# Kernel optimization log

Measured on AMD Instinct MI355X. Metric: run time of the kernel, lower is better.

## Reference

```python
import jax, jax.numpy as jnp
import numpy as np

T, B, D, H = 512, 64, 512, 512


def setup_inputs() -> dict:
    key = jax.random.key(0)
    ks = jax.random.split(key, 9)
    s_in = 1.0 / np.sqrt(D + H)  # nn.Linear default init scale
    inputs = jax.random.normal(ks[0], (T, B, D), dtype=jnp.float32)
    def lin(kw, kb):
        W = jax.random.uniform(kw, (D + H, H), jnp.float32, -s_in, s_in)
        b = jax.random.uniform(kb, (H,), jnp.float32, -s_in, s_in)
        return W, b
    W_f, b_f = lin(ks[1], ks[2])
    W_i, b_i = lin(ks[3], ks[4])
    W_g, b_g = lin(ks[5], ks[6])
    W_o, b_o = lin(ks[7], ks[8])
    return {"inputs": inputs, "W_f": W_f, "b_f": b_f, "W_i": W_i, "b_i": b_i,
            "W_g": W_g, "b_g": b_g, "W_o": W_o, "b_o": b_o}


def reference(inputs, W_f, b_f, W_i, b_i, W_g, b_g, W_o, b_o):
    # inputs: [T, B, D]; weights: [D+H, H]; gate_factory is identity (default)
    Bsz = inputs.shape[1]
    Hd = W_f.shape[1]
    # Fuse the 4 gate linears into one [D+H, 4H] GEMM per step (same math).
    W = jnp.concatenate([W_f, W_i, W_g, W_o], axis=1)  # [D+H, 4H]
    b = jnp.concatenate([b_f, b_i, b_g, b_o], axis=0)  # [4H]
    h0 = jnp.zeros((Bsz, Hd), dtype=inputs.dtype)
    c0 = jnp.zeros((Bsz, Hd), dtype=inputs.dtype)

    def step(carry, x):
        hx, cx = carry
        combined = jnp.concatenate([x, hx], axis=1)        # [B, D+H]
        gates = combined @ W + b                            # [B, 4H]
        f, i, g, o = jnp.split(gates, 4, axis=1)
        f = jax.nn.sigmoid(f)
        i = jax.nn.sigmoid(i)
        g = jnp.tanh(g)
        o = jax.nn.sigmoid(o)
        cx = f * cx + i * g
        hx = o * jnp.tanh(cx)
        return (hx, cx), hx

    (hx, cx), outputs = jax.lax.scan(step, (h0, c0), inputs)
    return outputs, (hx, cx)
```

## Files before the change

### kernel.cpp

```cpp
#include <hip/hip_runtime.h>

typedef unsigned int u32;
typedef unsigned short u16;
typedef __attribute__((ext_vector_type(8))) short bf16x8;
typedef __attribute__((ext_vector_type(4))) float f32x4;

#define T_STEPS 512
#define NOUT_H  16777216ull
#define WS_FLAGS  256ull
#define WS_BIAS   8192ull
#define WS_HBUF0  16384ull
#define WS_HBUF1  81920ull
#define WS_WXS    147456ull
#define WS_WHS    2244608ull
#define WS_XC     4341760ull
#define WS_XW     37896192ull

__device__ __forceinline__ u16 f2bf(float f) {
  u32 u = __builtin_bit_cast(u32, f);
  u32 r = (u + 0x7fffu + ((u >> 16) & 1u)) >> 16;
  return (u16)r;
}
__device__ __forceinline__ float bf2f(u16 h) {
  u32 u = ((u32)h) << 16;
  return __builtin_bit_cast(float, u);
}
__device__ __forceinline__ float sigf(float x) {
  return __builtin_amdgcn_rcpf(1.0f + __expf(-x));
}
__device__ __forceinline__ float tanh_fast(float x) {
  float xc = fminf(15.0f, fmaxf(-15.0f, x));
  float e = __expf(2.0f * xc);
  return (e - 1.0f) * __builtin_amdgcn_rcpf(e + 1.0f);
}

__global__ void k_detect(const u32* __restrict__ x, u32* __restrict__ ws) {
  __shared__ int cnt;
  if (threadIdx.x == 0) cnt = 0;
  __syncthreads();
  int good = 0;
  for (int i = 0; i < 4; ++i) {
    u32 v = x[threadIdx.x * 4 + i];
    u32 e = (v >> 7) & 0xff;
    good += (e >= 100 && e <= 140) ? 1 : 0;
  }
  atomicAdd(&cnt, good);
  __syncthreads();
  if (threadIdx.x == 0) ws[0] = (cnt >= 512) ? 1u : 0u;
  u32* flags = ws + WS_FLAGS / 4;
  for (int i = threadIdx.x; i < 1024; i += 256) flags[i] = 0;
  u32* hb = ws + WS_HBUF0 / 4;
  for (int i = threadIdx.x; i < (131072 / 4); i += 256) hb[i] = 0;
}

__global__ void k_convx(const u32* __restrict__ ws, const void* __restrict__ xin,
                        u16* __restrict__ xc) {
  if (ws[0]) return;
  int idx = blockIdx.x * 256 + threadIdx.x;
  float4 f = ((const float4*)xin)[idx];
  ushort4 o;
  o.x = f2bf(f.x); o.y = f2bf(f.y); o.z = f2bf(f.z); o.w = f2bf(f.w);
  ((ushort4*)xc)[idx] = o;
}

__global__ void k_prepw(u32* __restrict__ ws,
                        const void* Wf, const void* Wi, const void* Wg, const void* Wo,
                        const void* bfp, const void* bip, const void* bgp, const void* bop) {
  u32 mode = ws[0];
  const void* Wp[4] = {Wf, Wi, Wg, Wo};
  int tid = blockIdx.x * 256 + threadIdx.x;
  u16* wxs = (u16*)((char*)ws + WS_WXS);
  u16* whs = (u16*)((char*)ws + WS_WHS);
  int c, iswh;
  if (tid < 131072) { c = tid; iswh = 0; } else { c = tid - 131072; iswh = 1; }
  int n = c & 15, q = (c >> 4) & 3, ks = (c >> 6) & 15;
  int g, j, krow0;
  if (!iswh) {
    int ntg = c >> 10;
    int col = ntg * 16 + n; g = col >> 9; j = col & 511; krow0 = 0;
  } else {
    int nt = (c >> 10) & 1, w = c >> 11;
    int cl = nt * 16 + n; g = cl >> 3; j = w * 8 + (cl & 7); krow0 = 512;
  }
  int kbase = krow0 + ks * 32 + q * 8;
  u16 vals[8];
  if (mode) {
    const u16* Ws = (const u16*)Wp[g];
    for (int jj = 0; jj < 8; ++jj) vals[jj] = Ws[(size_t)(kbase + jj) * 512 + j];
  } else {
    const float* Ws = (const float*)Wp[g];
    for (int jj = 0; jj < 8; ++jj) vals[jj] = f2bf(Ws[(size_t)(kbase + jj) * 512 + j]);
  }
  uint4 pk;
  pk.x = (u32)vals[0] | ((u32)vals[1] << 16);
  pk.y = (u32)vals[2] | ((u32)vals[3] << 16);
  pk.z = (u32)vals[4] | ((u32)vals[5] << 16);
  pk.w = (u32)vals[6] | ((u32)vals[7] << 16);
  ((uint4*)(iswh ? whs : wxs))[c] = pk;
  if (tid < 2048) {
    const void* bp[4] = {bfp, bip, bgp, bop};
    int bg = tid >> 9, bj = tid & 511;
    float* bias = (float*)((char*)ws + WS_BIAS);
    bias[tid] = mode ? bf2f(((const u16*)bp[bg])[bj]) : ((const float*)bp[bg])[bj];
  }
}

__global__ __launch_bounds__(256) void k_xw(u32* __restrict__ ws, const void* __restrict__ xorig,
                                            int xwf32) {
  u32 mode = ws[0];
  const u16* xc = mode ? (const u16*)xorig : (const u16*)((char*)ws + WS_XC);
  const u16* wxs = (const u16*)((char*)ws + WS_WXS);
  const float* bias = (const float*)((char*)ws + WS_BIAS);
  char* xwp = (char*)ws + WS_XW;
  int v = threadIdx.x >> 6, lane = threadIdx.x & 63, q = lane >> 4, n = lane & 15;
  int mg = blockIdx.x >> 4, ng = blockIdx.x & 15;
  f32x4 acc[4][2] = {};
  for (int ks = 0; ks < 16; ++ks) {
    bf16x8 a[4];
#pragma unroll
    for (int mt = 0; mt < 4; ++mt)
      a[mt] = *(const bf16x8*)(xc + ((size_t)(mg * 64 + mt * 16 + n) * 512 + ks * 32 + q * 8));
#pragma unroll
    for (int jb = 0; jb < 2; ++jb) {
      int ntg = ng * 8 + v * 2 + jb;
      bf16x8 b = *(const bf16x8*)(wxs + ((size_t)(ntg * 16 + ks) * 64 + lane) * 8);
#pragma unroll
      for (int mt = 0; mt < 4; ++mt)
        acc[mt][jb] = __builtin_amdgcn_mfma_f32_16x16x32_bf16(a[mt], b, acc[mt][jb], 0, 0, 0);
    }
  }
#pragma unroll
  for (int jb = 0; jb < 2; ++jb) {
    int ntg = ng * 8 + v * 2 + jb;
    int col = ntg * 16 + n;
    float bv = bias[col];
    int g = col >> 9, j = col & 511;
    int w = j >> 3, cl = g * 8 + (j & 7);
    int nt4 = cl >> 4, n4 = cl & 15;
#pragma unroll
    for (int mt = 0; mt < 4; ++mt) {
      size_t base = ((((size_t)mg * 4 + mt) * 64 + w) * 2 + nt4) * 64 + q * 16 + n4;
      f32x4 vec = acc[mt][jb];
      vec[0] += bv; vec[1] += bv; vec[2] += bv; vec[3] += bv;
      if (xwf32) {
        ((f32x4*)xwp)[base] = vec;
      } else {
        ushort4 o;
        o.x = f2bf(vec[0]); o.y = f2bf(vec[1]); o.z = f2bf(vec[2]); o.w = f2bf(vec[3]);
        ((ushort4*)xwp)[base] = o;
      }
    }
  }
}

__global__ __launch_bounds__(256, 1) void k_rec(u32* __restrict__ ws, void* __restrict__ out,
                                                int xwf32) {
  __shared__ __align__(16) u16 whlds[16384];
  __shared__ float gbuf[4 * 16 * 33];
  __shared__ __align__(16) u16 houtbuf[64 * 8];
  u32 mode = ws[0];
  u32* flags = ws + WS_FLAGS / 4;
  const u16* whs = (const u16*)((char*)ws + WS_WHS);
  char* hb0 = (char*)ws + WS_HBUF0;
  char* hb1 = (char*)ws + WS_HBUF1;
  const char* xwp = (const char*)ws + WS_XW;
  int w = blockIdx.x, tid = threadIdx.x, v = tid >> 6, lane = tid & 63;
  int q = lane >> 4, n = lane & 15;

  {
    const uint4* src = (const uint4*)(whs + (size_t)w * 16384);
    uint4* dst = (uint4*)whlds;
    for (int i = tid; i < 2048; i += 256) dst[i] = src[i];
  }
  __syncthreads();

  float creg[2] = {0.f, 0.f};
  float* gb = &gbuf[v * 16 * 33];
  const u32* fp = flags + lane * 4;

  for (int t = 0; t < T_STEPS; ++t) {
    f32x4 xw0, xw1;
    {
      size_t b0 = ((((size_t)t * 4 + v) * 64 + w) * 2 + 0) * 64 + lane;
      if (xwf32) {
        xw0 = ((const f32x4*)xwp)[b0];
        xw1 = ((const f32x4*)xwp)[b0 + 64];
      } else {
        ushort4 a0 = ((const ushort4*)xwp)[b0];
        ushort4 a1 = ((const ushort4*)xwp)[b0 + 64];
        xw0[0] = bf2f(a0.x); xw0[1] = bf2f(a0.y); xw0[2] = bf2f(a0.z); xw0[3] = bf2f(a0.w);
        xw1[0] = bf2f(a1.x); xw1[1] = bf2f(a1.y); xw1[2] = bf2f(a1.z); xw1[3] = bf2f(a1.w);
      }
    }
    {
      u32 need = (u32)t;
      while (true) {
        uint4 f;
        asm volatile("global_load_dwordx4 %0, %1, off sc0 sc1\n\ts_waitcnt vmcnt(0)"
                     : "=&v"(f) : "v"(fp) : "memory");
        int ok = (f.x >= need) && (f.y >= need) && (f.z >= need) && (f.w >= need);
        if (__all(ok)) break;
        __builtin_amdgcn_s_sleep(1);
      }
    }
    const char* hcur = (t & 1) ? hb1 : hb0;
    char* hnxt = (t & 1) ? hb0 : hb1;

    uint4 ha[16];
    {
      const char* b0 = hcur + (size_t)v * 16384 + (size_t)lane * 16;
      const char* b4 = b0 + 4096;
      const char* b8 = b0 + 8192;
      const char* b12 = b0 + 12288;
      asm volatile(
          "global_load_dwordx4 %0, %16, off sc0 sc1\n\t"
          "global_load_dwordx4 %1, %16, off offset:1024 sc0 sc1\n\t"
          "global_load_dwordx4 %2, %16, off offset:2048 sc0 sc1\n\t"
          "global_load_dwordx4 %3, %16, off offset:3072 sc0 sc1\n\t"
          "global_load_dwordx4 %4, %17, off sc0 sc1\n\t"
          "global_load_dwordx4 %5, %17, off offset:1024 sc0 sc1\n\t"
          "global_load_dwordx4 %6, %17, off offset:2048 sc0 sc1\n\t"
          "global_load_dwordx4 %7, %17, off offset:3072 sc0 sc1\n\t"
          "global_load_dwordx4 %8, %18, off sc0 sc1\n\t"
          "global_load_dwordx4 %9, %18, off offset:1024 sc0 sc1\n\t"
          "global_load_dwordx4 %10, %18, off offset:2048 sc0 sc1\n\t"
          "global_load_dwordx4 %11, %18, off offset:3072 sc0 sc1\n\t"
          "global_load_dwordx4 %12, %19, off sc0 sc1\n\t"
          "global_load_dwordx4 %13, %19, off offset:1024 sc0 sc1\n\t"
          "global_load_dwordx4 %14, %19, off offset:2048 sc0 sc1\n\t"
          "global_load_dwordx4 %15, %19, off offset:3072 sc0 sc1\n\t"
          "s_waitcnt vmcnt(0)"
          : "=&v"(ha[0]), "=&v"(ha[1]), "=&v"(ha[2]), "=&v"(ha[3]),
            "=&v"(ha[4]), "=&v"(ha[5]), "=&v"(ha[6]), "=&v"(ha[7]),
            "=&v"(ha[8]), "=&v"(ha[9]), "=&v"(ha[10]), "=&v"(ha[11]),
            "=&v"(ha[12]), "=&v"(ha[13]), "=&v"(ha[14]), "=&v"(ha[15])
          : "v"(b0), "v"(b4), "v"(b8), "v"(b12)
          : "memory");
    }

    f32x4 acc0 = xw0, acc1 = xw1;
#pragma unroll
    for (int ks = 0; ks < 16; ++ks) {
      bf16x8 a = __builtin_bit_cast(bf16x8, ha[ks]);
      bf16x8 bb0 = *(const bf16x8*)&whlds[(ks * 64 + lane) * 8];
      bf16x8 bb1 = *(const bf16x8*)&whlds[((16 + ks) * 64 + lane) * 8];
      acc0 = __builtin_amdgcn_mfma_f32_16x16x32_bf16(a, bb0, acc0, 0, 0, 0);
      acc1 = __builtin_amdgcn_mfma_f32_16x16x32_bf16(a, bb1, acc1, 0, 0, 0);
    }
#pragma unroll
    for (int r = 0; r < 4; ++r) {
      gb[(q * 4 + r) * 33 + n] = acc0[r];
      gb[(q * 4 + r) * 33 + 16 + n] = acc1[r];
    }
    float hnew_s[2], cnew_s[2];
    int bidx[2];
#pragma unroll
    for (int it = 0; it < 2; ++it) {
      int item = it * 64 + lane, r16 = item >> 3, jj = item & 7, b = v * 16 + r16;
      float zf = gb[r16 * 33 + jj];
      float zi = gb[r16 * 33 + 8 + jj];
      float zg = gb[r16 * 33 + 16 + jj];
      float zo = gb[r16 * 33 + 24 + jj];
      float fg = sigf(zf), ig = sigf(zi), gg = tanh_fast(zg), og = sigf(zo);
      float cnew = fg * creg[it] + ig * gg;
      float hnew = og * tanh_fast(cnew);
      creg[it] = cnew;
      hnew_s[it] = hnew; cnew_s[it] = cnew; bidx[it] = b;
      houtbuf[b * 8 + jj] = f2bf(hnew);
    }
    if (lane < 16) {
      const u32* hv = (const u32*)&houtbuf[(v * 16 + lane) * 8];
      u32 v0 = hv[0], v1 = hv[1], v2 = hv[2], v3 = hv[3];
      size_t ci = (((size_t)v * 16 + (w >> 2)) * 4 + (w & 3)) * 16 + lane;
      void* dst = hnxt + ci * 16;
      asm volatile(
          "global_store_dword %0, %1, off sc0 sc1\n\t"
          "global_store_dword %0, %2, off offset:4 sc0 sc1\n\t"
          "global_store_dword %0, %3, off offset:8 sc0 sc1\n\t"
          "global_store_dword %0, %4, off offset:12 sc0 sc1"
          :: "v"(dst), "v"(v0), "v"(v1), "v"(v2), "v"(v3) : "memory");
    }
    asm volatile("s_waitcnt vmcnt(0)" ::: "memory");
    if (lane == 0) {
      u32 tag = (u32)(t + 1);
      u32* fdst = flags + (w * 4 + v);
      asm volatile("global_store_dword %0, %1, off sc0 sc1" :: "v"(fdst), "v"(tag) : "memory");
    }
#pragma unroll
    for (int it = 0; it < 2; ++it) {
      int item = it * 64 + lane, jj = item & 7, b = bidx[it];
      size_t oi = ((size_t)t * 64 + b) * 512 + w * 8 + jj;
      if (mode) ((u16*)out)[oi] = f2bf(hnew_s[it]); else ((float*)out)[oi] = hnew_s[it];
      if (t == T_STEPS - 1) {
        size_t hx = NOUT_H + (size_t)b * 512 + w * 8 + jj;
        if (mode) { ((u16*)out)[hx] = f2bf(hnew_s[it]); ((u16*)out)[hx + 32768] = f2bf(cnew_s[it]); }
        else      { ((float*)out)[hx] = hnew_s[it]; ((float*)out)[hx + 32768] = cnew_s[it]; }
      }
    }
  }
}

extern "C" void kernel_launch(void* const* d_in, const int* in_sizes, int n_in,
                              void* d_out, int out_size, void* d_ws, size_t ws_size,
                              hipStream_t stream) {
  const void* X = d_in[0];
  u32* ws = (u32*)d_ws;
  int xwf32 = (ws_size >= (size_t)(WS_XW + 268435456ull + 1024ull)) ? 1 : 0;

  k_detect<<<1, 256, 0, stream>>>((const u32*)X, ws);
  k_convx<<<16384, 256, 0, stream>>>(ws, X, (u16*)((char*)d_ws + WS_XC));
  k_prepw<<<1024, 256, 0, stream>>>(ws, d_in[1], d_in[3], d_in[5], d_in[7],
                                    d_in[2], d_in[4], d_in[6], d_in[8]);
  k_xw<<<8192, 256, 0, stream>>>(ws, X, xwf32);
  k_rec<<<64, 256, 0, stream>>>(ws, d_out, xwf32);
}
```

Baseline: 2.316 ms.

## Keep recurrent weights in registers, shuffle gates, and tighten per-step sync

The recurrent weight slice is held in VGPRs instead of LDS, and the gate values are exchanged between lanes with cross-lane shuffles, so the LDS staging buffers and their round trips go away. The MFMA chain is split into two independent accumulators to shorten the dependency chain. The flag poll now loads one dword per lane and no longer sleeps between polls. The next step's input projection is prefetched after the flag store, and h is written straight to global memory with short stores. The cost is much higher register pressure and more polling traffic on the flags.

```diff
diff --git a/kernel.cpp b/kernel.cpp
--- a/kernel.cpp
+++ b/kernel.cpp
@@ -155,9 +155,6 @@
 
 __global__ __launch_bounds__(256, 1) void k_rec(u32* __restrict__ ws, void* __restrict__ out,
                                                 int xwf32) {
-  __shared__ __align__(16) u16 whlds[16384];
-  __shared__ float gbuf[4 * 16 * 33];
-  __shared__ __align__(16) u16 houtbuf[64 * 8];
   u32 mode = ws[0];
   u32* flags = ws + WS_FLAGS / 4;
   const u16* whs = (const u16*)((char*)ws + WS_WHS);
@@ -166,41 +163,42 @@
   const char* xwp = (const char*)ws + WS_XW;
   int w = blockIdx.x, tid = threadIdx.x, v = tid >> 6, lane = tid & 63;
   int q = lane >> 4, n = lane & 15;
-
+  int hi = (n >> 3) & 1;
+  int r0 = hi ? 2 : 0;
+  int jj = n & 7;
+
+  bf16x8 bfr[2][16];
+#pragma unroll
+  for (int nt = 0; nt < 2; ++nt)
+#pragma unroll
+    for (int ks = 0; ks < 16; ++ks)
+      bfr[nt][ks] = *(const bf16x8*)(whs + ((size_t)w * 2048 + nt * 1024 + ks * 64 + lane) * 8);
+
+  float creg[2] = {0.f, 0.f};
+  u32* fp = flags + lane * 4 + v;
+
+  f32x4 xw0, xw1;
   {
-    const uint4* src = (const uint4*)(whs + (size_t)w * 16384);
-    uint4* dst = (uint4*)whlds;
-    for (int i = tid; i < 2048; i += 256) dst[i] = src[i];
-  }
-  __syncthreads();
-
-  float creg[2] = {0.f, 0.f};
-  float* gb = &gbuf[v * 16 * 33];
-  const u32* fp = flags + lane * 4;
+    size_t b0 = ((((size_t)0 * 4 + v) * 64 + w) * 2 + 0) * 64 + lane;
+    if (xwf32) {
+      xw0 = ((const f32x4*)xwp)[b0];
+      xw1 = ((const f32x4*)xwp)[b0 + 64];
+    } else {
+      ushort4 a0 = ((const ushort4*)xwp)[b0];
+      ushort4 a1 = ((const ushort4*)xwp)[b0 + 64];
+      xw0[0] = bf2f(a0.x); xw0[1] = bf2f(a0.y); xw0[2] = bf2f(a0.z); xw0[3] = bf2f(a0.w);
+      xw1[0] = bf2f(a1.x); xw1[1] = bf2f(a1.y); xw1[2] = bf2f(a1.z); xw1[3] = bf2f(a1.w);
+    }
+  }
 
   for (int t = 0; t < T_STEPS; ++t) {
-    f32x4 xw0, xw1;
-    {
-      size_t b0 = ((((size_t)t * 4 + v) * 64 + w) * 2 + 0) * 64 + lane;
-      if (xwf32) {
-        xw0 = ((const f32x4*)xwp)[b0];
-        xw1 = ((const f32x4*)xwp)[b0 + 64];
-      } else {
-        ushort4 a0 = ((const ushort4*)xwp)[b0];
-        ushort4 a1 = ((const ushort4*)xwp)[b0 + 64];
-        xw0[0] = bf2f(a0.x); xw0[1] = bf2f(a0.y); xw0[2] = bf2f(a0.z); xw0[3] = bf2f(a0.w);
-        xw1[0] = bf2f(a1.x); xw1[1] = bf2f(a1.y); xw1[2] = bf2f(a1.z); xw1[3] = bf2f(a1.w);
-      }
-    }
     {
       u32 need = (u32)t;
       while (true) {
-        uint4 f;
-        asm volatile("global_load_dwordx4 %0, %1, off sc0 sc1\n\ts_waitcnt vmcnt(0)"
+        u32 f;
+        asm volatile("global_load_dword %0, %1, off sc0 sc1\n\ts_waitcnt vmcnt(0)"
                      : "=&v"(f) : "v"(fp) : "memory");
-        int ok = (f.x >= need) && (f.y >= need) && (f.z >= need) && (f.w >= need);
-        if (__all(ok)) break;
-        __builtin_amdgcn_s_sleep(1);
+        if (__all((int)(f >= need))) break;
       }
     }
     const char* hcur = (t & 1) ? hb1 : hb0;
@@ -238,47 +236,50 @@
           : "memory");
     }
 
-    f32x4 acc0 = xw0, acc1 = xw1;
-#pragma unroll
-    for (int ks = 0; ks < 16; ++ks) {
-      bf16x8 a = __builtin_bit_cast(bf16x8, ha[ks]);
-      bf16x8 bb0 = *(const bf16x8*)&whlds[(ks * 64 + lane) * 8];
-      bf16x8 bb1 = *(const bf16x8*)&whlds[((16 + ks) * 64 + lane) * 8];
-      acc0 = __builtin_amdgcn_mfma_f32_16x16x32_bf16(a, bb0, acc0, 0, 0, 0);
-      acc1 = __builtin_amdgcn_mfma_f32_16x16x32_bf16(a, bb1, acc1, 0, 0, 0);
-    }
-#pragma unroll
-    for (int r = 0; r < 4; ++r) {
-      gb[(q * 4 + r) * 33 + n] = acc0[r];
-      gb[(q * 4 + r) * 33 + 16 + n] = acc1[r];
-    }
+    f32x4 a0a = xw0, a1a = xw1;
+    f32x4 a0b = {0.f, 0.f, 0.f, 0.f}, a1b = {0.f, 0.f, 0.f, 0.f};
+#pragma unroll
+    for (int ks = 0; ks < 8; ++ks) {
+      bf16x8 aA = __builtin_bit_cast(bf16x8, ha[ks]);
+      bf16x8 aB = __builtin_bit_cast(bf16x8, ha[8 + ks]);
+      a0a = __builtin_amdgcn_mfma_f32_16x16x32_bf16(aA, bfr[0][ks], a0a, 0, 0, 0);
+      a1a = __builtin_amdgcn_mfma_f32_16x16x32_bf16(aA, bfr[1][ks], a1a, 0, 0, 0);
+      a0b = __builtin_amdgcn_mfma_f32_16x16x32_bf16(aB, bfr[0][8 + ks], a0b, 0, 0, 0);
+      a1b = __builtin_amdgcn_mfma_f32_16x16x32_bf16(aB, bfr[1][8 + ks], a1b, 0, 0, 0);
+    }
+    f32x4 acc0 = a0a + a0b, acc1 = a1a + a1b;
+
+    float t00 = __shfl_xor(hi ? acc0[0] : acc0[2], 8, 64);
+    float t01 = __shfl_xor(hi ? acc0[1] : acc0[3], 8, 64);
+    float t20 = __shfl_xor(hi ? acc1[0] : acc1[2], 8, 64);
+    float t21 = __shfl_xor(hi ? acc1[1] : acc1[3], 8, 64);
+
     float hnew_s[2], cnew_s[2];
-    int bidx[2];
+    u32 h16_s[2];
 #pragma unroll
     for (int it = 0; it < 2; ++it) {
-      int item = it * 64 + lane, r16 = item >> 3, jj = item & 7, b = v * 16 + r16;
-      float zf = gb[r16 * 33 + jj];
-      float zi = gb[r16 * 33 + 8 + jj];
-      float zg = gb[r16 * 33 + 16 + jj];
-      float zo = gb[r16 * 33 + 24 + jj];
+      int r = r0 + it;
+      float tx0 = it ? t01 : t00;
+      float tx2 = it ? t21 : t20;
+      float zf = hi ? tx0 : acc0[it];
+      float zi = hi ? acc0[r] : tx0;
+      float zg = hi ? tx2 : acc1[it];
+      float zo = hi ? acc1[r] : tx2;
       float fg = sigf(zf), ig = sigf(zi), gg = tanh_fast(zg), og = sigf(zo);
       float cnew = fg * creg[it] + ig * gg;
       float hnew = og * tanh_fast(cnew);
       creg[it] = cnew;
-      hnew_s[it] = hnew; cnew_s[it] = cnew; bidx[it] = b;
-      houtbuf[b * 8 + jj] = f2bf(hnew);
-    }
-    if (lane < 16) {
-      const u32* hv = (const u32*)&houtbuf[(v * 16 + lane) * 8];
-      u32 v0 = hv[0], v1 = hv[1], v2 = hv[2], v3 = hv[3];
-      size_t ci = (((size_t)v * 16 + (w >> 2)) * 4 + (w & 3)) * 16 + lane;
-      void* dst = hnxt + ci * 16;
+      hnew_s[it] = hnew; cnew_s[it] = cnew;
+      h16_s[it] = (u32)f2bf(hnew);
+    }
+
+    {
+      size_t ci0 = ((((size_t)v * 16 + (w >> 2)) * 4 + (w & 3)) * 16 + (q * 4 + r0));
+      char* dst = hnxt + ci0 * 16 + jj * 2;
       asm volatile(
-          "global_store_dword %0, %1, off sc0 sc1\n\t"
-          "global_store_dword %0, %2, off offset:4 sc0 sc1\n\t"
-          "global_store_dword %0, %3, off offset:8 sc0 sc1\n\t"
-          "global_store_dword %0, %4, off offset:12 sc0 sc1"
-          :: "v"(dst), "v"(v0), "v"(v1), "v"(v2), "v"(v3) : "memory");
+          "global_store_short %0, %1, off sc0 sc1\n\t"
+          "global_store_short %0, %2, off offset:16 sc0 sc1"
+          :: "v"(dst), "v"(h16_s[0]), "v"(h16_s[1]) : "memory");
     }
     asm volatile("s_waitcnt vmcnt(0)" ::: "memory");
     if (lane == 0) {
@@ -286,14 +287,28 @@
       u32* fdst = flags + (w * 4 + v);
       asm volatile("global_store_dword %0, %1, off sc0 sc1" :: "v"(fdst), "v"(tag) : "memory");
     }
+
+    {
+      int tn = (t + 1 < T_STEPS) ? t + 1 : t;
+      size_t b0 = ((((size_t)tn * 4 + v) * 64 + w) * 2 + 0) * 64 + lane;
+      if (xwf32) {
+        xw0 = ((const f32x4*)xwp)[b0];
+        xw1 = ((const f32x4*)xwp)[b0 + 64];
+      } else {
+        ushort4 a0 = ((const ushort4*)xwp)[b0];
+        ushort4 a1 = ((const ushort4*)xwp)[b0 + 64];
+        xw0[0] = bf2f(a0.x); xw0[1] = bf2f(a0.y); xw0[2] = bf2f(a0.z); xw0[3] = bf2f(a0.w);
+        xw1[0] = bf2f(a1.x); xw1[1] = bf2f(a1.y); xw1[2] = bf2f(a1.z); xw1[3] = bf2f(a1.w);
+      }
+    }
 #pragma unroll
     for (int it = 0; it < 2; ++it) {
-      int item = it * 64 + lane, jj = item & 7, b = bidx[it];
+      int b = v * 16 + q * 4 + r0 + it;
       size_t oi = ((size_t)t * 64 + b) * 512 + w * 8 + jj;
-      if (mode) ((u16*)out)[oi] = f2bf(hnew_s[it]); else ((float*)out)[oi] = hnew_s[it];
+      if (mode) ((u16*)out)[oi] = (u16)h16_s[it]; else ((float*)out)[oi] = hnew_s[it];
       if (t == T_STEPS - 1) {
         size_t hx = NOUT_H + (size_t)b * 512 + w * 8 + jj;
-        if (mode) { ((u16*)out)[hx] = f2bf(hnew_s[it]); ((u16*)out)[hx + 32768] = f2bf(cnew_s[it]); }
+        if (mode) { ((u16*)out)[hx] = (u16)h16_s[it]; ((u16*)out)[hx + 32768] = f2bf(cnew_s[it]); }
         else      { ((float*)out)[hx] = hnew_s[it]; ((float*)out)[hx + 32768] = cnew_s[it]; }
       }
     }
```

New measurement: 2.819 ms. +21.7%, slower.
